# Optimization experiments

Measured on AMD Instinct MI355X. Metric: run time of the kernel, lower is better.

## Reference

```python
import jax, jax.numpy as jnp
import numpy as np

N, E = 50000, 800000
H, C = 4, 32          # heads, per-head channels
IN_DIM = 128
NEG_SLOPE = 0.2


def gat_conv(x, edge_index, W, a_src, a_dst, b):
    """PyG-style GATConv: Wx, per-edge leaky-relu logits, dst-segment softmax,
    scatter-weighted aggregation, concat heads, add bias. Self-loops added."""
    n = x.shape[0]
    loops = jnp.arange(n, dtype=edge_index.dtype)
    src = jnp.concatenate([edge_index[0], loops])
    dst = jnp.concatenate([edge_index[1], loops])
    xw = (x @ W).reshape(n, H, C)                      # [N,H,C]
    alpha_src = jnp.sum(xw * a_src, axis=-1)           # [N,H]
    alpha_dst = jnp.sum(xw * a_dst, axis=-1)           # [N,H]
    e = jax.nn.leaky_relu(alpha_src[src] + alpha_dst[dst], NEG_SLOPE)  # [E+N,H]
    m = jax.ops.segment_max(e, dst, num_segments=n)    # stable softmax per dst
    e = jnp.exp(e - m[dst])
    denom = jax.ops.segment_sum(e, dst, num_segments=n)
    alpha = e / denom[dst]                             # [E+N,H]
    out = jax.ops.segment_sum(alpha[:, :, None] * xw[src], dst, num_segments=n)
    return out.reshape(n, H * C) + b


def setup_inputs() -> dict:
    key = jax.random.key(0)
    ks = jax.random.split(key, 12)
    HC = H * C
    x = jax.random.normal(ks[0], (N, IN_DIM), dtype=jnp.float32)
    edge_index = jax.random.randint(ks[1], (2, E), 0, N, dtype=jnp.int32)
    s0 = 1.0 / np.sqrt(IN_DIM)
    s1 = 1.0 / np.sqrt(HC)
    return {
        "x": x,
        "edge_index": edge_index,
        "W0": jax.random.normal(ks[2], (IN_DIM, HC), dtype=jnp.float32) * s0,
        "a_src0": jax.random.normal(ks[3], (H, C), dtype=jnp.float32) * s1,
        "a_dst0": jax.random.normal(ks[4], (H, C), dtype=jnp.float32) * s1,
        "b0": jnp.zeros((HC,), dtype=jnp.float32),
        "W1": jax.random.normal(ks[5], (HC, HC), dtype=jnp.float32) * s1,
        "a_src1": jax.random.normal(ks[6], (H, C), dtype=jnp.float32) * s1,
        "a_dst1": jax.random.normal(ks[7], (H, C), dtype=jnp.float32) * s1,
        "b1": jnp.zeros((HC,), dtype=jnp.float32),
        "Wr": jax.random.normal(ks[8], (HC, 1), dtype=jnp.float32) * s1,
        "br": jnp.zeros((1,), dtype=jnp.float32),
    }


def reference(x, edge_index, W0, a_src0, a_dst0, b0, W1, a_src1, a_dst1, b1, Wr, br):
    h = jax.nn.elu(gat_conv(x, edge_index, W0, a_src0, a_dst0, b0))
    # F.dropout(training=False) -> identity (eval mode)
    h = jax.nn.elu(gat_conv(h, edge_index, W1, a_src1, a_dst1, b1))
    return h @ Wr + br
```

## Files before the change

kernel.cpp:

```cpp
#include <hip/hip_runtime.h>
#include <hip/hip_bf16.h>
#include <hip/hip_fp16.h>

#define DEV __device__ __forceinline__

DEV float lrelu(float x) { return x > 0.f ? x : 0.2f * x; }
DEV float elu(float x)   { return x > 0.f ? x : __expf(x) - 1.f; }

#define CAP 64

__global__ __launch_bounds__(256, 5)
void scatter_gemm0(const int* __restrict__ ei, int* __restrict__ deg,
                   int* __restrict__ col2, int E, int sblk,
                   const float* __restrict__ X, const float* __restrict__ W,
                   const float* __restrict__ a_src, const float* __restrict__ a_dst,
                   __half2* __restrict__ xw2, float* __restrict__ asrc,
                   float* __restrict__ adst, int n) {
    if ((int)blockIdx.x < sblk) {
        int stride = sblk * 256;
        for (int e = blockIdx.x * 256 + threadIdx.x; e < E; e += stride) {
            int s = ei[e], d = ei[E + e];
            int pos = atomicAdd(&deg[d], 1);
            if (pos < CAP) col2[d * CAP + pos] = s;
        }
        return;
    }
    __shared__ float Xs[32][68];
    __shared__ float Ws[32][132];
    int t = threadIdx.x;
    int n0 = ((int)blockIdx.x - sblk) * 64;
    int rg = t >> 4;
    int cg = t & 15;
    int q0 = cg * 8 + ((cg >= 8) ? 4 : 0);

    float acc[4][8];
#pragma unroll
    for (int r = 0; r < 4; ++r)
#pragma unroll
        for (int c = 0; c < 8; ++c) acc[r][c] = 0.f;

    float4 px[2], pw[4];
    auto load_x = [&](int k0, float4* p) {
#pragma unroll
        for (int it = 0; it < 2; ++it) {
            int idx = t + it * 256;
            int row = idx >> 3, kq = idx & 7;
            int gr = n0 + row;
            p[it] = (gr < n) ? *(const float4*)&X[(size_t)gr * 128 + k0 + kq * 4]
                             : make_float4(0.f, 0.f, 0.f, 0.f);
        }
    };
    auto load_w = [&](int k0, float4* p) {
#pragma unroll
        for (int it = 0; it < 4; ++it) {
            int idx = t + it * 256;
            int k = idx >> 5, cq = idx & 31;
            p[it] = *(const float4*)&W[(size_t)(k0 + k) * 128 + cq * 4];
        }
    };
    auto store_lds = [&](const float4* pX, const float4* pW) {
#pragma unroll
        for (int it = 0; it < 2; ++it) {
            int idx = t + it * 256;
            int row = idx >> 3, kq = idx & 7;
            Xs[kq * 4 + 0][row] = pX[it].x;
            Xs[kq * 4 + 1][row] = pX[it].y;
            Xs[kq * 4 + 2][row] = pX[it].z;
            Xs[kq * 4 + 3][row] = pX[it].w;
        }
#pragma unroll
        for (int it = 0; it < 4; ++it) {
            int idx = t + it * 256;
            int k = idx >> 5, cq = idx & 31;
            *(float4*)&Ws[k][cq * 4 + ((cq >= 16) ? 4 : 0)] = pW[it];
        }
    };

    load_x(0, px);
    load_w(0, pw);
    for (int c4 = 0; c4 < 4; ++c4) {
        store_lds(px, pw);
        __syncthreads();
        if (c4 < 3) { load_x((c4 + 1) * 32, px); load_w((c4 + 1) * 32, pw); }
#pragma unroll 4
        for (int k = 0; k < 32; ++k) {
            float4 xv = *(const float4*)&Xs[k][rg * 4];
            float4 w0 = *(const float4*)&Ws[k][q0];
            float4 w1 = *(const float4*)&Ws[k][q0 + 4];
            float xr[4] = {xv.x, xv.y, xv.z, xv.w};
            float wr[8] = {w0.x, w0.y, w0.z, w0.w, w1.x, w1.y, w1.z, w1.w};
#pragma unroll
            for (int r = 0; r < 4; ++r)
#pragma unroll
                for (int c = 0; c < 8; ++c)
                    acc[r][c] = fmaf(xr[r], wr[c], acc[r][c]);
        }
        __syncthreads();
    }

    int c0 = cg * 8;
    int h = cg >> 2;
    float as8[8], ad8[8];
#pragma unroll
    for (int c = 0; c < 8; ++c) { as8[c] = a_src[c0 + c]; ad8[c] = a_dst[c0 + c]; }
#pragma unroll
    for (int r = 0; r < 4; ++r) {
        int gr = n0 + rg * 4 + r;
        float s_ = 0.f, d_ = 0.f;
#pragma unroll
        for (int c = 0; c < 8; ++c) {
            s_ = fmaf(acc[r][c], as8[c], s_);
            d_ = fmaf(acc[r][c], ad8[c], d_);
        }
        s_ += __shfl_xor(s_, 1); s_ += __shfl_xor(s_, 2);
        d_ += __shfl_xor(d_, 1); d_ += __shfl_xor(d_, 2);
        if (gr < n) {
            __half2* rowp = &xw2[(size_t)gr * 64 + (c0 >> 1)];
            rowp[0] = __floats2half2_rn(acc[r][0], acc[r][1]);
            rowp[1] = __floats2half2_rn(acc[r][2], acc[r][3]);
            rowp[2] = __floats2half2_rn(acc[r][4], acc[r][5]);
            rowp[3] = __floats2half2_rn(acc[r][6], acc[r][7]);
            if ((t & 3) == 0) { asrc[gr * 4 + h] = s_; adst[gr * 4 + h] = d_; }
        }
    }
}

__global__ __launch_bounds__(256, 5)
void gemm_alpha_v6(const float* __restrict__ X, const float* __restrict__ W,
                   const float* __restrict__ a_src, const float* __restrict__ a_dst,
                   __half2* __restrict__ xw2, float* __restrict__ asrc,
                   float* __restrict__ adst, int n) {
    __shared__ float Xs[32][68];
    __shared__ float Ws[32][132];
    int t = threadIdx.x;
    int n0 = blockIdx.x * 64;
    int rg = t >> 4;
    int cg = t & 15;
    int q0 = cg * 8 + ((cg >= 8) ? 4 : 0);

    float acc[4][8];
#pragma unroll
    for (int r = 0; r < 4; ++r)
#pragma unroll
        for (int c = 0; c < 8; ++c) acc[r][c] = 0.f;

    float4 px[2], pw[4];
    auto load_x = [&](int k0, float4* p) {
#pragma unroll
        for (int it = 0; it < 2; ++it) {
            int idx = t + it * 256;
            int row = idx >> 3, kq = idx & 7;
            int gr = n0 + row;
            p[it] = (gr < n) ? *(const float4*)&X[(size_t)gr * 128 + k0 + kq * 4]
                             : make_float4(0.f, 0.f, 0.f, 0.f);
        }
    };
    auto load_w = [&](int k0, float4* p) {
#pragma unroll
        for (int it = 0; it < 4; ++it) {
            int idx = t + it * 256;
            int k = idx >> 5, cq = idx & 31;
            p[it] = *(const float4*)&W[(size_t)(k0 + k) * 128 + cq * 4];
        }
    };
    auto store_lds = [&](const float4* pX, const float4* pW) {
#pragma unroll
        for (int it = 0; it < 2; ++it) {
            int idx = t + it * 256;
            int row = idx >> 3, kq = idx & 7;
            Xs[kq * 4 + 0][row] = pX[it].x;
            Xs[kq * 4 + 1][row] = pX[it].y;
            Xs[kq * 4 + 2][row] = pX[it].z;
            Xs[kq * 4 + 3][row] = pX[it].w;
        }
#pragma unroll
        for (int it = 0; it < 4; ++it) {
            int idx = t + it * 256;
            int k = idx >> 5, cq = idx & 31;
            *(float4*)&Ws[k][cq * 4 + ((cq >= 16) ? 4 : 0)] = pW[it];
        }
    };

    load_x(0, px);
    load_w(0, pw);
    for (int c4 = 0; c4 < 4; ++c4) {
        store_lds(px, pw);
        __syncthreads();
        if (c4 < 3) { load_x((c4 + 1) * 32, px); load_w((c4 + 1) * 32, pw); }
#pragma unroll 4
        for (int k = 0; k < 32; ++k) {
            float4 xv = *(const float4*)&Xs[k][rg * 4];
            float4 w0 = *(const float4*)&Ws[k][q0];
            float4 w1 = *(const float4*)&Ws[k][q0 + 4];
            float xr[4] = {xv.x, xv.y, xv.z, xv.w};
            float wr[8] = {w0.x, w0.y, w0.z, w0.w, w1.x, w1.y, w1.z, w1.w};
#pragma unroll
            for (int r = 0; r < 4; ++r)
#pragma unroll
                for (int c = 0; c < 8; ++c)
                    acc[r][c] = fmaf(xr[r], wr[c], acc[r][c]);
        }
        __syncthreads();
    }

    int c0 = cg * 8;
    int h = cg >> 2;
    float as8[8], ad8[8];
#pragma unroll
    for (int c = 0; c < 8; ++c) { as8[c] = a_src[c0 + c]; ad8[c] = a_dst[c0 + c]; }
#pragma unroll
    for (int r = 0; r < 4; ++r) {
        int gr = n0 + rg * 4 + r;
        float s_ = 0.f, d_ = 0.f;
#pragma unroll
        for (int c = 0; c < 8; ++c) {
            s_ = fmaf(acc[r][c], as8[c], s_);
            d_ = fmaf(acc[r][c], ad8[c], d_);
        }
        s_ += __shfl_xor(s_, 1); s_ += __shfl_xor(s_, 2);
        d_ += __shfl_xor(d_, 1); d_ += __shfl_xor(d_, 2);
        if (gr < n) {
            __half2* rowp = &xw2[(size_t)gr * 64 + (c0 >> 1)];
            rowp[0] = __floats2half2_rn(acc[r][0], acc[r][1]);
            rowp[1] = __floats2half2_rn(acc[r][2], acc[r][3]);
            rowp[2] = __floats2half2_rn(acc[r][4], acc[r][5]);
            rowp[3] = __floats2half2_rn(acc[r][6], acc[r][7]);
            if ((t & 3) == 0) { asrc[gr * 4 + h] = s_; adst[gr * 4 + h] = d_; }
        }
    }
}

__global__ __launch_bounds__(256, 8)
void aggregate_v7(const __half2* __restrict__ xw2, const float* __restrict__ asrc,
                  const float* __restrict__ adst, const int* __restrict__ col2,
                  const int* __restrict__ deg, const float* __restrict__ bias,
                  float* __restrict__ out128, float* __restrict__ out1,
                  const float* __restrict__ Wr, const float* __restrict__ br, int n) {
    int l = threadIdx.x & 63;
    int i = __builtin_amdgcn_readfirstlane((blockIdx.x * 256 + threadIdx.x) >> 6);
    if (i >= n) return;
    int h4 = l & 3;
    int jj = l >> 2;
    int hA = l >> 4;
    int beg = i * CAP;
    int dcount = deg[i]; if (dcount > CAP) dcount = CAP;
    int end = beg + dcount;
    float ad = adst[i * 4 + h4];
    float wsum = __expf(lrelu(asrc[i * 4 + h4] + ad));
    float wselfA = __shfl(wsum, hA);
    float2 row_i = __half22float2(xw2[(size_t)i * 64 + l]);
    float2 a0 = make_float2(wselfA * row_i.x, wselfA * row_i.y);
    float2 a1 = make_float2(0.f, 0.f);
    float2 a2 = make_float2(0.f, 0.f);
    float2 a3 = make_float2(0.f, 0.f);

    int ce = beg;
    for (; ce + 16 <= end; ce += 16) {
        int s = col2[ce + jj];
        float wv = __expf(lrelu(asrc[s * 4 + h4] + ad));
        float sv = wv;
        sv += __shfl_xor(sv, 4);
        sv += __shfl_xor(sv, 8);
        sv += __shfl_xor(sv, 16);
        sv += __shfl_xor(sv, 32);
        wsum += sv;
#pragma unroll
        for (int j = 0; j < 16; j += 4) {
            int s0 = col2[ce + j + 0];
            int s1 = col2[ce + j + 1];
            int s2 = col2[ce + j + 2];
            int s3 = col2[ce + j + 3];
            float g0 = __shfl(wv, (j + 0) * 4 + hA);
            float g1 = __shfl(wv, (j + 1) * 4 + hA);
            float g2 = __shfl(wv, (j + 2) * 4 + hA);
            float g3 = __shfl(wv, (j + 3) * 4 + hA);
            float2 v0 = __half22float2(xw2[(size_t)s0 * 64 + l]);
            float2 v1 = __half22float2(xw2[(size_t)s1 * 64 + l]);
            float2 v2 = __half22float2(xw2[(size_t)s2 * 64 + l]);
            float2 v3 = __half22float2(xw2[(size_t)s3 * 64 + l]);
            a0.x = fmaf(g0, v0.x, a0.x); a0.y = fmaf(g0, v0.y, a0.y);
            a1.x = fmaf(g1, v1.x, a1.x); a1.y = fmaf(g1, v1.y, a1.y);
            a2.x = fmaf(g2, v2.x, a2.x); a2.y = fmaf(g2, v2.y, a2.y);
            a3.x = fmaf(g3, v3.x, a3.x); a3.y = fmaf(g3, v3.y, a3.y);
        }
    }
    if (ce < end) {
        int nc = end - ce;
        float wv = 0.f;
        if (jj < nc) {
            int s = col2[ce + jj];
            wv = __expf(lrelu(asrc[s * 4 + h4] + ad));
        }
        float sv = wv;
        sv += __shfl_xor(sv, 4);
        sv += __shfl_xor(sv, 8);
        sv += __shfl_xor(sv, 16);
        sv += __shfl_xor(sv, 32);
        wsum += sv;
#pragma unroll
        for (int j = 0; j < 16; ++j) {
            if (j >= nc) break;
            int sj = col2[ce + j];
            float wg = __shfl(wv, j * 4 + hA);
            float2 v = __half22float2(xw2[(size_t)sj * 64 + l]);
            a0.x = fmaf(wg, v.x, a0.x);
            a0.y = fmaf(wg, v.y, a0.y);
        }
    }
    a0.x += (a1.x + a2.x) + a3.x;
    a0.y += (a1.y + a2.y) + a3.y;
    float wsA = __shfl(wsum, hA);
    float inv = 1.f / wsA;
    float2 bv = *(const float2*)&bias[2 * l];
    float rx = elu(a0.x * inv + bv.x);
    float ry = elu(a0.y * inv + bv.y);
    if (out1 == nullptr) {
        *(float2*)&out128[(size_t)i * 128 + 2 * l] = make_float2(rx, ry);
    } else {
        float v = rx * Wr[2 * l] + ry * Wr[2 * l + 1];
#pragma unroll
        for (int off = 32; off > 0; off >>= 1) v += __shfl_xor(v, off);
        if (l == 0) out1[i] = v + br[0];
    }
}

extern "C" void kernel_launch(void* const* d_in, const int* in_sizes, int n_in,
                              void* d_out, int out_size, void* d_ws, size_t ws_size,
                              hipStream_t stream) {
    const float* x   = (const float*)d_in[0];
    const int*   ei  = (const int*)d_in[1];
    const float* W0  = (const float*)d_in[2];
    const float* as0 = (const float*)d_in[3];
    const float* ad0 = (const float*)d_in[4];
    const float* b0  = (const float*)d_in[5];
    const float* W1  = (const float*)d_in[6];
    const float* as1 = (const float*)d_in[7];
    const float* ad1 = (const float*)d_in[8];
    const float* b1  = (const float*)d_in[9];
    const float* Wr  = (const float*)d_in[10];
    const float* br  = (const float*)d_in[11];
    float* out = (float*)d_out;

    const int N = in_sizes[0] / 128;
    const int E = in_sizes[1] / 2;

    char* w = (char*)d_ws;
    size_t off = 0;
    auto alloc = [&](size_t bytes) -> void* {
        void* p = w + off;
        off += (bytes + 255) & ~size_t(255);
        return p;
    };
    __half2* xw2  = (__half2*)alloc((size_t)N * 64 * 4);
    float* bufB   = (float*)alloc((size_t)N * 128 * 4);
    float* asrc   = (float*)alloc((size_t)N * 4 * 4);
    float* adst   = (float*)alloc((size_t)N * 4 * 4);
    int*   deg    = (int*)alloc((size_t)N * 4);
    int*   col2   = (int*)alloc((size_t)N * CAP * 4);

    hipMemsetAsync(deg, 0, (size_t)N * 4, stream);

    const int sblk = 768;
    const int gblk = (N + 63) / 64;
    const int ablk = (N + 3) / 4;
    scatter_gemm0<<<sblk + gblk, 256, 0, stream>>>(ei, deg, col2, E, sblk,
                                                   x, W0, as0, ad0, xw2, asrc, adst, N);
    aggregate_v7<<<ablk, 256, 0, stream>>>(xw2, asrc, adst, col2, deg, b0, bufB,
                                           nullptr, nullptr, nullptr, N);
    gemm_alpha_v6<<<gblk, 256, 0, stream>>>(bufB, W1, as1, ad1, xw2, asrc, adst, N);
    aggregate_v7<<<ablk, 256, 0, stream>>>(xw2, asrc, adst, col2, deg, b1, nullptr,
                                           out, Wr, br, N);
}
```

Before: 294.5 us.

## Fuse layer-0 aggregation with layer-1 GEMM via LDS staging

Merges the first aggregation kernel and the second GEMM into one 512-thread kernel. Each block aggregates 64 destination rows into a transposed LDS tile and multiplies it by W1 directly, so the fp32 N×128 intermediate is never written to or read back from global memory. The first kernel is also reordered so GEMM blocks come before the scatter blocks, and xw/alpha buffers are split per layer so the fused kernel never reads and writes the same buffer. In exchange, only 782 large blocks run the irregular gather phase, which can lower parallelism and latency hiding compared with the former 12.5k-block aggregate launch.

```diff
diff --git a/kernel.cpp b/kernel.cpp
--- a/kernel.cpp
+++ b/kernel.cpp
@@ -10,15 +10,16 @@
 #define CAP 64
 
 __global__ __launch_bounds__(256, 5)
-void scatter_gemm0(const int* __restrict__ ei, int* __restrict__ deg,
-                   int* __restrict__ col2, int E, int sblk,
-                   const float* __restrict__ X, const float* __restrict__ W,
+void gemm0_scatter(const float* __restrict__ X, const float* __restrict__ W,
                    const float* __restrict__ a_src, const float* __restrict__ a_dst,
                    __half2* __restrict__ xw2, float* __restrict__ asrc,
-                   float* __restrict__ adst, int n) {
-    if ((int)blockIdx.x < sblk) {
+                   float* __restrict__ adst, int n, int gblk,
+                   const int* __restrict__ ei, int* __restrict__ deg,
+                   int* __restrict__ col2, int E, int sblk) {
+    if ((int)blockIdx.x >= gblk) {
         int stride = sblk * 256;
-        for (int e = blockIdx.x * 256 + threadIdx.x; e < E; e += stride) {
+        for (int e = ((int)blockIdx.x - gblk) * 256 + (int)threadIdx.x; e < E;
+             e += stride) {
             int s = ei[e], d = ei[E + e];
             int pos = atomicAdd(&deg[d], 1);
             if (pos < CAP) col2[d * CAP + pos] = s;
@@ -28,7 +29,7 @@
     __shared__ float Xs[32][68];
     __shared__ float Ws[32][132];
     int t = threadIdx.x;
-    int n0 = ((int)blockIdx.x - sblk) * 64;
+    int n0 = (int)blockIdx.x * 64;
     int rg = t >> 4;
     int cg = t & 15;
     int q0 = cg * 8 + ((cg >= 8) ? 4 : 0);
@@ -125,80 +126,151 @@
     }
 }
 
-__global__ __launch_bounds__(256, 5)
-void gemm_alpha_v6(const float* __restrict__ X, const float* __restrict__ W,
-                   const float* __restrict__ a_src, const float* __restrict__ a_dst,
-                   __half2* __restrict__ xw2, float* __restrict__ asrc,
-                   float* __restrict__ adst, int n) {
-    __shared__ float Xs[32][68];
+__global__ __launch_bounds__(512, 6)
+void agg0_gemm1(const __half2* __restrict__ xw2a, const float* __restrict__ asrc0,
+                const float* __restrict__ adst0, const int* __restrict__ col2,
+                const int* __restrict__ deg, const float* __restrict__ bias,
+                const float* __restrict__ W, const float* __restrict__ a_src,
+                const float* __restrict__ a_dst, __half2* __restrict__ xw2b,
+                float* __restrict__ asrc1, float* __restrict__ adst1, int n) {
+    __shared__ float Xh[128 * 66];
     __shared__ float Ws[32][132];
     int t = threadIdx.x;
-    int n0 = blockIdx.x * 64;
+    int n0 = (int)blockIdx.x * 64;
+    int l = t & 63;
+    int q = t >> 6;
+
+    {
+        int h4 = l & 3;
+        int jj = l >> 2;
+        int hA = l >> 4;
+        for (int it = 0; it < 8; ++it) {
+            int i = __builtin_amdgcn_readfirstlane(n0 + q * 8 + it);
+            float rx = 0.f, ry = 0.f;
+            if (i < n) {
+                int beg = i * CAP;
+                int dcount = deg[i]; if (dcount > CAP) dcount = CAP;
+                int end = beg + dcount;
+                float ad = adst0[i * 4 + h4];
+                float wsum = __expf(lrelu(asrc0[i * 4 + h4] + ad));
+                float wselfA = __shfl(wsum, hA);
+                float2 row_i = __half22float2(xw2a[(size_t)i * 64 + l]);
+                float2 a0 = make_float2(wselfA * row_i.x, wselfA * row_i.y);
+                float2 a1 = make_float2(0.f, 0.f);
+                float2 a2 = make_float2(0.f, 0.f);
+                float2 a3 = make_float2(0.f, 0.f);
+                int ce = beg;
+                for (; ce + 16 <= end; ce += 16) {
+                    int s = col2[ce + jj];
+                    float wv = __expf(lrelu(asrc0[s * 4 + h4] + ad));
+                    float sv = wv;
+                    sv += __shfl_xor(sv, 4);
+                    sv += __shfl_xor(sv, 8);
+                    sv += __shfl_xor(sv, 16);
+                    sv += __shfl_xor(sv, 32);
+                    wsum += sv;
+#pragma unroll
+                    for (int j = 0; j < 16; j += 4) {
+                        int s0 = col2[ce + j + 0];
+                        int s1 = col2[ce + j + 1];
+                        int s2 = col2[ce + j + 2];
+                        int s3 = col2[ce + j + 3];
+                        float g0 = __shfl(wv, (j + 0) * 4 + hA);
+                        float g1 = __shfl(wv, (j + 1) * 4 + hA);
+                        float g2 = __shfl(wv, (j + 2) * 4 + hA);
+                        float g3 = __shfl(wv, (j + 3) * 4 + hA);
+                        float2 v0 = __half22float2(xw2a[(size_t)s0 * 64 + l]);
+                        float2 v1 = __half22float2(xw2a[(size_t)s1 * 64 + l]);
+                        float2 v2 = __half22float2(xw2a[(size_t)s2 * 64 + l]);
+                        float2 v3 = __half22float2(xw2a[(size_t)s3 * 64 + l]);
+                        a0.x = fmaf(g0, v0.x, a0.x); a0.y = fmaf(g0, v0.y, a0.y);
+                        a1.x = fmaf(g1, v1.x, a1.x); a1.y = fmaf(g1, v1.y, a1.y);
+                        a2.x = fmaf(g2, v2.x, a2.x); a2.y = fmaf(g2, v2.y, a2.y);
+                        a3.x = fmaf(g3, v3.x, a3.x); a3.y = fmaf(g3, v3.y, a3.y);
+                    }
+                }
+                if (ce < end) {
+                    int nc = end - ce;
+                    float wv = 0.f;
+                    if (jj < nc) {
+                        int s = col2[ce + jj];
+                        wv = __expf(lrelu(asrc0[s * 4 + h4] + ad));
+                    }
+                    float sv = wv;
+                    sv += __shfl_xor(sv, 4);
+                    sv += __shfl_xor(sv, 8);
+                    sv += __shfl_xor(sv, 16);
+                    sv += __shfl_xor(sv, 32);
+                    wsum += sv;
+#pragma unroll
+                    for (int j = 0; j < 16; ++j) {
+                        if (j >= nc) break;
+                        int sj = col2[ce + j];
+                        float wg = __shfl(wv, j * 4 + hA);
+                        float2 v = __half22float2(xw2a[(size_t)sj * 64 + l]);
+                        a0.x = fmaf(wg, v.x, a0.x);
+                        a0.y = fmaf(wg, v.y, a0.y);
+                    }
+                }
+                a0.x += (a1.x + a2.x) + a3.x;
+                a0.y += (a1.y + a2.y) + a3.y;
+                float wsA = __shfl(wsum, hA);
+                float inv = 1.f / wsA;
+                float2 bv = *(const float2*)&bias[2 * l];
+                rx = elu(a0.x * inv + bv.x);
+                ry = elu(a0.y * inv + bv.y);
+            }
+            int row = q * 8 + it;
+            Xh[(2 * l) * 66 + row]     = rx;
+            Xh[(2 * l + 1) * 66 + row] = ry;
+        }
+    }
+    __syncthreads();
+
     int rg = t >> 4;
     int cg = t & 15;
     int q0 = cg * 8 + ((cg >= 8) ? 4 : 0);
-
-    float acc[4][8];
-#pragma unroll
-    for (int r = 0; r < 4; ++r)
+    float acc[2][8];
+#pragma unroll
+    for (int r = 0; r < 2; ++r)
 #pragma unroll
         for (int c = 0; c < 8; ++c) acc[r][c] = 0.f;
 
-    float4 px[2], pw[4];
-    auto load_x = [&](int k0, float4* p) {
+    float4 pw[2];
+    auto load_w = [&](int k0, float4* p) {
 #pragma unroll
         for (int it = 0; it < 2; ++it) {
-            int idx = t + it * 256;
-            int row = idx >> 3, kq = idx & 7;
-            int gr = n0 + row;
-            p[it] = (gr < n) ? *(const float4*)&X[(size_t)gr * 128 + k0 + kq * 4]
-                             : make_float4(0.f, 0.f, 0.f, 0.f);
-        }
-    };
-    auto load_w = [&](int k0, float4* p) {
-#pragma unroll
-        for (int it = 0; it < 4; ++it) {
-            int idx = t + it * 256;
+            int idx = t + it * 512;
             int k = idx >> 5, cq = idx & 31;
             p[it] = *(const float4*)&W[(size_t)(k0 + k) * 128 + cq * 4];
         }
     };
-    auto store_lds = [&](const float4* pX, const float4* pW) {
+    auto store_w = [&](const float4* p) {
 #pragma unroll
         for (int it = 0; it < 2; ++it) {
-            int idx = t + it * 256;
-            int row = idx >> 3, kq = idx & 7;
-            Xs[kq * 4 + 0][row] = pX[it].x;
-            Xs[kq * 4 + 1][row] = pX[it].y;
-            Xs[kq * 4 + 2][row] = pX[it].z;
-            Xs[kq * 4 + 3][row] = pX[it].w;
-        }
-#pragma unroll
-        for (int it = 0; it < 4; ++it) {
-            int idx = t + it * 256;
+            int idx = t + it * 512;
             int k = idx >> 5, cq = idx & 31;
-            *(float4*)&Ws[k][cq * 4 + ((cq >= 16) ? 4 : 0)] = pW[it];
-        }
-    };
-
-    load_x(0, px);
+            *(float4*)&Ws[k][cq * 4 + ((cq >= 16) ? 4 : 0)] = p[it];
+        }
+    };
+
     load_w(0, pw);
     for (int c4 = 0; c4 < 4; ++c4) {
-        store_lds(px, pw);
+        store_w(pw);
         __syncthreads();
-        if (c4 < 3) { load_x((c4 + 1) * 32, px); load_w((c4 + 1) * 32, pw); }
+        if (c4 < 3) load_w((c4 + 1) * 32, pw);
+        int kb = c4 * 32;
 #pragma unroll 4
         for (int k = 0; k < 32; ++k) {
-            float4 xv = *(const float4*)&Xs[k][rg * 4];
+            float2 xv = *(const float2*)&Xh[(kb + k) * 66 + rg * 2];
             float4 w0 = *(const float4*)&Ws[k][q0];
             float4 w1 = *(const float4*)&Ws[k][q0 + 4];
-            float xr[4] = {xv.x, xv.y, xv.z, xv.w};
             float wr[8] = {w0.x, w0.y, w0.z, w0.w, w1.x, w1.y, w1.z, w1.w};
 #pragma unroll
-            for (int r = 0; r < 4; ++r)
-#pragma unroll
-                for (int c = 0; c < 8; ++c)
-                    acc[r][c] = fmaf(xr[r], wr[c], acc[r][c]);
+            for (int c = 0; c < 8; ++c) {
+                acc[0][c] = fmaf(xv.x, wr[c], acc[0][c]);
+                acc[1][c] = fmaf(xv.y, wr[c], acc[1][c]);
+            }
         }
         __syncthreads();
     }
@@ -209,8 +281,8 @@
 #pragma unroll
     for (int c = 0; c < 8; ++c) { as8[c] = a_src[c0 + c]; ad8[c] = a_dst[c0 + c]; }
 #pragma unroll
-    for (int r = 0; r < 4; ++r) {
-        int gr = n0 + rg * 4 + r;
+    for (int r = 0; r < 2; ++r) {
+        int gr = n0 + rg * 2 + r;
         float s_ = 0.f, d_ = 0.f;
 #pragma unroll
         for (int c = 0; c < 8; ++c) {
@@ -220,12 +292,12 @@
         s_ += __shfl_xor(s_, 1); s_ += __shfl_xor(s_, 2);
         d_ += __shfl_xor(d_, 1); d_ += __shfl_xor(d_, 2);
         if (gr < n) {
-            __half2* rowp = &xw2[(size_t)gr * 64 + (c0 >> 1)];
+            __half2* rowp = &xw2b[(size_t)gr * 64 + (c0 >> 1)];
             rowp[0] = __floats2half2_rn(acc[r][0], acc[r][1]);
             rowp[1] = __floats2half2_rn(acc[r][2], acc[r][3]);
             rowp[2] = __floats2half2_rn(acc[r][4], acc[r][5]);
             rowp[3] = __floats2half2_rn(acc[r][6], acc[r][7]);
-            if ((t & 3) == 0) { asrc[gr * 4 + h] = s_; adst[gr * 4 + h] = d_; }
+            if ((t & 3) == 0) { asrc1[gr * 4 + h] = s_; adst1[gr * 4 + h] = d_; }
         }
     }
 }
@@ -234,8 +306,8 @@
 void aggregate_v7(const __half2* __restrict__ xw2, const float* __restrict__ asrc,
                   const float* __restrict__ adst, const int* __restrict__ col2,
                   const int* __restrict__ deg, const float* __restrict__ bias,
-                  float* __restrict__ out128, float* __restrict__ out1,
-                  const float* __restrict__ Wr, const float* __restrict__ br, int n) {
+                  float* __restrict__ out1, const float* __restrict__ Wr,
+                  const float* __restrict__ br, int n) {
     int l = threadIdx.x & 63;
     int i = __builtin_amdgcn_readfirstlane((blockIdx.x * 256 + threadIdx.x) >> 6);
     if (i >= n) return;
@@ -314,14 +386,10 @@
     float2 bv = *(const float2*)&bias[2 * l];
     float rx = elu(a0.x * inv + bv.x);
     float ry = elu(a0.y * inv + bv.y);
-    if (out1 == nullptr) {
-        *(float2*)&out128[(size_t)i * 128 + 2 * l] = make_float2(rx, ry);
-    } else {
-        float v = rx * Wr[2 * l] + ry * Wr[2 * l + 1];
-#pragma unroll
-        for (int off = 32; off > 0; off >>= 1) v += __shfl_xor(v, off);
-        if (l == 0) out1[i] = v + br[0];
-    }
+    float v = rx * Wr[2 * l] + ry * Wr[2 * l + 1];
+#pragma unroll
+    for (int off = 32; off > 0; off >>= 1) v += __shfl_xor(v, off);
+    if (l == 0) out1[i] = v + br[0];
 }
 
 extern "C" void kernel_launch(void* const* d_in, const int* in_sizes, int n_in,
@@ -351,23 +419,25 @@
         off += (bytes + 255) & ~size_t(255);
         return p;
     };
-    __half2* xw2  = (__half2*)alloc((size_t)N * 64 * 4);
-    float* bufB   = (float*)alloc((size_t)N * 128 * 4);
-    float* asrc   = (float*)alloc((size_t)N * 4 * 4);
-    float* adst   = (float*)alloc((size_t)N * 4 * 4);
-    int*   deg    = (int*)alloc((size_t)N * 4);
-    int*   col2   = (int*)alloc((size_t)N * CAP * 4);
+    __half2* xw2a  = (__half2*)alloc((size_t)N * 64 * 4);
+    __half2* xw2b  = (__half2*)alloc((size_t)N * 64 * 4);
+    float* asrc0   = (float*)alloc((size_t)N * 4 * 4);
+    float* adst0   = (float*)alloc((size_t)N * 4 * 4);
+    float* asrc1   = (float*)alloc((size_t)N * 4 * 4);
+    float* adst1   = (float*)alloc((size_t)N * 4 * 4);
+    int*   deg     = (int*)alloc((size_t)N * 4);
+    int*   col2    = (int*)alloc((size_t)N * CAP * 4);
 
     hipMemsetAsync(deg, 0, (size_t)N * 4, stream);
 
+    const int gblk = (N + 63) / 64;
     const int sblk = 768;
-    const int gblk = (N + 63) / 64;
     const int ablk = (N + 3) / 4;
-    scatter_gemm0<<<sblk + gblk, 256, 0, stream>>>(ei, deg, col2, E, sblk,
-                                                   x, W0, as0, ad0, xw2, asrc, adst, N);
-    aggregate_v7<<<ablk, 256, 0, stream>>>(xw2, asrc, adst, col2, deg, b0, bufB,
-                                           nullptr, nullptr, nullptr, N);
-    gemm_alpha_v6<<<gblk, 256, 0, stream>>>(bufB, W1, as1, ad1, xw2, asrc, adst, N);
-    aggregate_v7<<<ablk, 256, 0, stream>>>(xw2, asrc, adst, col2, deg, b1, nullptr,
+    gemm0_scatter<<<gblk + sblk, 256, 0, stream>>>(x, W0, as0, ad0, xw2a, asrc0,
+                                                   adst0, N, gblk, ei, deg, col2,
+                                                   E, sblk);
+    agg0_gemm1<<<gblk, 512, 0, stream>>>(xw2a, asrc0, adst0, col2, deg, b0,
+                                         W1, as1, ad1, xw2b, asrc1, adst1, N);
+    aggregate_v7<<<ablk, 256, 0, stream>>>(xw2b, asrc1, adst1, col2, deg, b1,
                                            out, Wr, br, N);
 }
```

Result: slower. 314.5 us (+6.8%).
